# Performance work log

Hardware: AMD Instinct MI355X
Metric: run time of the kernel (lower is better)

Reference implementation:

```python
import jax, jax.numpy as jnp
import numpy as np
import math

B, N, F_IN, F_OUT = 2, 2048, 32, 32
R, LEV = 2, 2
SIGMA = 1.0


def setup_inputs() -> dict:
    key = jax.random.key(0)
    k1, k2, k3, k4 = jax.random.split(key, 4)
    x = jax.random.normal(k1, (B, N, F_IN), dtype=jnp.float32)
    # framelet decomposition operator, scaled so bmm outputs stay O(1)
    d_list = jax.random.normal(k2, (B, R * LEV * N, N + 1), dtype=jnp.float32) * (1.0 / math.sqrt(N))
    weight = jax.random.normal(k3, (F_IN, F_OUT), dtype=jnp.float32) * math.sqrt(2.0 / (F_IN + F_OUT))
    filt = jax.random.uniform(k4, (R * LEV * N, 1), dtype=jnp.float32, minval=0.9, maxval=1.1)
    bias = jnp.zeros((F_OUT,), dtype=jnp.float32)
    return {"x": x, "d_list": d_list, "weight": weight, "filt": filt, "bias": bias}


def reference(x, d_list, weight, filt, bias):
    num_nodes = x.shape[1]
    # dense feature transform
    xw = jnp.einsum('bnf,fo->bno', x, weight)
    # analysis: drop first column of d_list, bmm with transformed features
    y = d_list[:, :, 1:]                       # [B, r*Lev*N, N]
    xc = jnp.einsum('bmn,bno->bmo', y, xw)     # [B, r*Lev*N, F_OUT]
    xc = filt[None, :, :] * xc                 # learned diagonal filter
    # In the original, ms_idx is reset to 0 every loop iteration, so only
    # ms[0] (== 1.0 by construction in multiScales) is ever used as the scale.
    thr = math.sqrt(2.0 * math.log(num_nodes)) / math.sqrt(num_nodes) * SIGMA
    low = xc[:, (LEV - 1) * num_nodes:LEV * num_nodes, :]   # low-pass block, kept
    high = xc[:, LEV * num_nodes:, :]                        # high-freq blocks
    # soft threshold: sign(x)*(|x|-thr+||x|-thr|)/2 == sign(x)*relu(|x|-thr)
    high = jnp.sign(high) * jnp.maximum(jnp.abs(high) - thr, jnp.float32(0.0))
    x_shrink = jnp.concatenate([low, high], axis=1)          # [B, (r*Lev-1)*N, F_OUT]
    # synthesis: crop first node-block, raw reshape (not transpose!) as in original
    d_crop = d_list[:, num_nodes:, :]                        # [B, (r*Lev-1)*N, N+1]
    y2 = d_crop.reshape(d_crop.shape[0], num_nodes + 1, -1)  # [B, N+1, (r*Lev-1)*N]
    out = jnp.einsum('bkm,bmo->bko', y2, x_shrink) + bias    # [B, N+1, F_OUT]
    return out
```

## Files before the change

### kernel.cpp

```cpp
#include <hip/hip_runtime.h>
#include <math.h>


#define DP 2049
#define THRS 0.08628973f

typedef float  f32x4  __attribute__((ext_vector_type(4)));
typedef float  f32x16 __attribute__((ext_vector_type(16)));
typedef short  s16x8  __attribute__((ext_vector_type(8)));
typedef unsigned short u16;

#define XWT_H 0u
#define XWT_L 262144u
#define XST_H 524288u
#define XST_L 1310720u
#define P1_B  2097152u
#define P2_B  14680064u

union U8 { unsigned u[4]; s16x8 v; };

__device__ __forceinline__ unsigned cvtpk(float a, float b) {
  unsigned r;
  asm("v_cvt_pk_bf16_f32 %0, %1, %2" : "=v"(r) : "v"(a), "v"(b));
  return r;
}
__device__ __forceinline__ void split2(float a0, float a1, unsigned& h, unsigned& l) {
  h = cvtpk(a0, a1);
  const float f0 = __uint_as_float(h << 16);
  const float f1 = __uint_as_float(h & 0xFFFF0000u);
  l = cvtpk(a0 - f0, a1 - f1);
}
__device__ __forceinline__ f32x4 ld4u(const float* p) {
  f32x4 r; __builtin_memcpy(&r, p, 16); return r;
}

__global__ __launch_bounds__(256) void k_pre(const float* __restrict__ x,
                                             const float* __restrict__ wgt,
                                             u16* __restrict__ xwt_h,
                                             u16* __restrict__ xwt_l) {
  const int idx = blockIdx.x * 256 + threadIdx.x;
  const int n0  = (idx & 255) * 8;
  const int col = (idx >> 8) & 31;
  const int b   = idx >> 13;
  const float* xr = x + ((size_t)b * 2048 + n0) * 32;
  float acc[8];
#pragma unroll
  for (int j = 0; j < 8; ++j) acc[j] = 0.f;
#pragma unroll 8
  for (int f = 0; f < 32; ++f) {
    const float wf = wgt[f * 32 + col];
#pragma unroll
    for (int j = 0; j < 8; ++j) acc[j] = fmaf(xr[j * 32 + f], wf, acc[j]);
  }
  U8 H, L;
#pragma unroll
  for (int p = 0; p < 4; ++p) split2(acc[2 * p], acc[2 * p + 1], H.u[p], L.u[p]);
  const size_t o = ((size_t)b * 32 + col) * 2048 + n0;
  *(s16x8*)(xwt_h + o) = H.v;
  *(s16x8*)(xwt_l + o) = L.v;
}

__global__ __launch_bounds__(256, 4) void k_pass1(const float* __restrict__ dlist,
                                                  const u16* __restrict__ xwt_h,
                                                  const u16* __restrict__ xwt_l,
                                                  const float* __restrict__ filt,
                                                  float* __restrict__ p1) {
  const int mt = blockIdx.x, b = blockIdx.y, s = blockIdx.z;
  const int tid = threadIdx.x, wv = tid >> 6, lane = tid & 63;
  const int rc = lane & 31, oct = lane >> 5;
  const int m_a = mt * 128 + wv * 32 + rc;
  const int k0 = s * 256;

  const float* A  = dlist + ((size_t)(b * 8192 + 2048 + m_a)) * DP + 1 + k0 + oct * 8;
  const u16*   Bh = xwt_h + ((size_t)b * 32 + rc) * 2048 + k0 + oct * 8;
  const u16*   Bl = xwt_l + ((size_t)b * 32 + rc) * 2048 + k0 + oct * 8;

  f32x16 acc = {0.f,0.f,0.f,0.f,0.f,0.f,0.f,0.f,0.f,0.f,0.f,0.f,0.f,0.f,0.f,0.f};
#pragma unroll 2
  for (int st = 0; st < 16; ++st) {
    const f32x4 a0 = ld4u(A + st * 16);
    const f32x4 a1 = ld4u(A + st * 16 + 4);
    U8 Ah, Al;
    split2(a0.x, a0.y, Ah.u[0], Al.u[0]);
    split2(a0.z, a0.w, Ah.u[1], Al.u[1]);
    split2(a1.x, a1.y, Ah.u[2], Al.u[2]);
    split2(a1.z, a1.w, Ah.u[3], Al.u[3]);
    const s16x8 bh = *(const s16x8*)(Bh + st * 16);
    const s16x8 bl = *(const s16x8*)(Bl + st * 16);
    acc = __builtin_amdgcn_mfma_f32_32x32x16_bf16(Ah.v, bh, acc, 0, 0, 0);
    acc = __builtin_amdgcn_mfma_f32_32x32x16_bf16(Al.v, bh, acc, 0, 0, 0);
    acc = __builtin_amdgcn_mfma_f32_32x32x16_bf16(Ah.v, bl, acc, 0, 0, 0);
  }

  float* pc = p1 + ((size_t)((s * 2 + b) * 32 + rc)) * 6144 + mt * 128 + wv * 32 + 4 * oct;
  const float* fb = filt + 2048 + mt * 128 + wv * 32 + 4 * oct;
#pragma unroll
  for (int g = 0; g < 4; ++g) {
    const f32x4 fv = *(const f32x4*)(fb + 8 * g);
    f32x4 v;
    v.x = acc[4 * g + 0] * fv.x; v.y = acc[4 * g + 1] * fv.y;
    v.z = acc[4 * g + 2] * fv.z; v.w = acc[4 * g + 3] * fv.w;
    *(f32x4*)(pc + 8 * g) = v;
  }
}

__global__ __launch_bounds__(256) void k_shrink(const float* __restrict__ p1,
                                                u16* __restrict__ xst_h,
                                                u16* __restrict__ xst_l) {
  const int idx = blockIdx.x * 256 + threadIdx.x;
  const int m0  = (idx % 768) * 8;
  const int col = (idx / 768) % 32;
  const int b   = idx / 24576;
  f32x4 s0 = {0.f,0.f,0.f,0.f}, s1 = {0.f,0.f,0.f,0.f};
#pragma unroll
  for (int s = 0; s < 8; ++s) {
    const float* pr = p1 + ((size_t)((s * 2 + b) * 32 + col)) * 6144 + m0;
    const f32x4 v0 = *(const f32x4*)pr;
    const f32x4 v1 = *(const f32x4*)(pr + 4);
    s0 += v0; s1 += v1;
  }
  float a[8] = {s0.x, s0.y, s0.z, s0.w, s1.x, s1.y, s1.z, s1.w};
  if (m0 >= 2048) {
#pragma unroll
    for (int j = 0; j < 8; ++j) {
      const float t = fabsf(a[j]) - THRS;
      a[j] = t > 0.f ? copysignf(t, a[j]) : 0.f;
    }
  }
  U8 H, L;
#pragma unroll
  for (int p = 0; p < 4; ++p) split2(a[2 * p], a[2 * p + 1], H.u[p], L.u[p]);
  const size_t o = ((size_t)b * 32 + col) * 6144 + m0;
  *(s16x8*)(xst_h + o) = H.v;
  *(s16x8*)(xst_l + o) = L.v;
}

__global__ __launch_bounds__(256, 4) void k_pass2(const float* __restrict__ dlist,
                                                  const u16* __restrict__ xst_h,
                                                  const u16* __restrict__ xst_l,
                                                  float* __restrict__ p2) {
  const int kt = blockIdx.x, b = blockIdx.y, s = blockIdx.z;
  const int tid = threadIdx.x, wv = tid >> 6, lane = tid & 63;
  const int rc = lane & 31, oct = lane >> 5;
  int krow = kt * 128 + wv * 32 + rc;
  if (krow > 2048) krow = 2048;
  const int m0 = s * 256;

  const float* A  = dlist + (size_t)b * 8192 * DP + (size_t)2048 * DP
                  + (size_t)krow * 6144 + m0 + oct * 8;
  const u16*   Bh = xst_h + ((size_t)b * 32 + rc) * 6144 + m0 + oct * 8;
  const u16*   Bl = xst_l + ((size_t)b * 32 + rc) * 6144 + m0 + oct * 8;

  f32x16 acc = {0.f,0.f,0.f,0.f,0.f,0.f,0.f,0.f,0.f,0.f,0.f,0.f,0.f,0.f,0.f,0.f};
#pragma unroll 2
  for (int st = 0; st < 16; ++st) {
    const f32x4 a0 = *(const f32x4*)(A + st * 16);
    const f32x4 a1 = *(const f32x4*)(A + st * 16 + 4);
    U8 Ah, Al;
    split2(a0.x, a0.y, Ah.u[0], Al.u[0]);
    split2(a0.z, a0.w, Ah.u[1], Al.u[1]);
    split2(a1.x, a1.y, Ah.u[2], Al.u[2]);
    split2(a1.z, a1.w, Ah.u[3], Al.u[3]);
    const s16x8 bh = *(const s16x8*)(Bh + st * 16);
    const s16x8 bl = *(const s16x8*)(Bl + st * 16);
    acc = __builtin_amdgcn_mfma_f32_32x32x16_bf16(Ah.v, bh, acc, 0, 0, 0);
    acc = __builtin_amdgcn_mfma_f32_32x32x16_bf16(Al.v, bh, acc, 0, 0, 0);
    acc = __builtin_amdgcn_mfma_f32_32x32x16_bf16(Ah.v, bl, acc, 0, 0, 0);
  }

  float* pc = p2 + ((size_t)((s * 2 + b) * 32 + rc)) * 2176 + kt * 128 + wv * 32 + 4 * oct;
#pragma unroll
  for (int g = 0; g < 4; ++g) {
    f32x4 v;
    v.x = acc[4 * g + 0]; v.y = acc[4 * g + 1];
    v.z = acc[4 * g + 2]; v.w = acc[4 * g + 3];
    *(f32x4*)(pc + 8 * g) = v;
  }
}

__global__ __launch_bounds__(256) void k_reduce(const float* __restrict__ p2,
                                                const float* __restrict__ bias,
                                                float* __restrict__ out) {
  const int idx = blockIdx.x * 256 + threadIdx.x;
  if (idx >= 34816) return;
  const int k4  = idx % 544;
  const int col = (idx / 544) % 32;
  const int b   = idx / 17408;
  const int k0r = k4 * 4;
  f32x4 sum = {0.f,0.f,0.f,0.f};
#pragma unroll 8
  for (int s = 0; s < 24; ++s)
    sum += *(const f32x4*)(p2 + ((size_t)((s * 2 + b) * 32 + col)) * 2176 + k0r);
  const float bv = bias[col];
#pragma unroll
  for (int j = 0; j < 4; ++j) {
    const int k = k0r + j;
    if (k <= 2048) out[((size_t)b * 2049 + k) * 32 + col] = sum[j] + bv;
  }
}

extern "C" void kernel_launch(void* const* d_in, const int* in_sizes, int n_in,
                              void* d_out, int out_size, void* d_ws, size_t ws_size,
                              hipStream_t stream) {
  const float* x     = (const float*)d_in[0];
  const float* dlist = (const float*)d_in[1];
  const float* wgt   = (const float*)d_in[2];
  const float* filt  = (const float*)d_in[3];
  const float* bias  = (const float*)d_in[4];
  float* out = (float*)d_out;
  char*  ws  = (char*)d_ws;
  u16*   xwt_h = (u16*)(ws + XWT_H);
  u16*   xwt_l = (u16*)(ws + XWT_L);
  u16*   xst_h = (u16*)(ws + XST_H);
  u16*   xst_l = (u16*)(ws + XST_L);
  float* p1    = (float*)(ws + P1_B);
  float* p2    = (float*)(ws + P2_B);

  k_pre   <<<dim3(64),         dim3(256), 0, stream>>>(x, wgt, xwt_h, xwt_l);
  k_pass1 <<<dim3(48, 2, 8),   dim3(256), 0, stream>>>(dlist, xwt_h, xwt_l, filt, p1);
  k_shrink<<<dim3(192),        dim3(256), 0, stream>>>(p1, xst_h, xst_l);
  k_pass2 <<<dim3(17, 2, 24),  dim3(256), 0, stream>>>(dlist, xst_h, xst_l, p2);
  k_reduce<<<dim3(136),        dim3(256), 0, stream>>>(p2, bias, out);
}
```

Baseline: 269.5 us.

## Stage d_list tiles through LDS with async global_load_lds and packed B layout

Both GEMM passes now copy the d_list A operand into swizzled, double-buffered shared memory using global_load_lds. Each wave therefore reads rows with coalesced accesses instead of strided per-lane vector loads. The bf16 hi/lo B operands are stored pre-packed in MFMA fragment order so each lane does one contiguous load. Split-K counts rise from 8 to 16 and from 24 to 32, which adds parallelism but also makes the partial-sum reductions and workspace larger.

After: 257.8 us. -4.4%, faster.

```diff
diff --git a/kernel.cpp b/kernel.cpp
--- a/kernel.cpp
+++ b/kernel.cpp
@@ -10,12 +10,12 @@
 typedef short  s16x8  __attribute__((ext_vector_type(8)));
 typedef unsigned short u16;
 
-#define XWT_H 0u
-#define XWT_L 262144u
-#define XST_H 524288u
-#define XST_L 1310720u
+#define XWP_H 0u
+#define XWP_L 262144u
+#define XSP_H 524288u
+#define XSP_L 1310720u
 #define P1_B  2097152u
-#define P2_B  14680064u
+#define P2_B  27262976u
 
 union U8 { unsigned u[4]; s16x8 v; };
 
@@ -30,14 +30,19 @@
   const float f1 = __uint_as_float(h & 0xFFFF0000u);
   l = cvtpk(a0 - f0, a1 - f1);
 }
-__device__ __forceinline__ f32x4 ld4u(const float* p) {
-  f32x4 r; __builtin_memcpy(&r, p, 16); return r;
+__device__ __forceinline__ void cp4(const float* g, float* l) {
+  __builtin_amdgcn_global_load_lds((const __attribute__((address_space(1))) void*)g,
+                                   (__attribute__((address_space(3))) void*)l, 4, 0, 0);
+}
+__device__ __forceinline__ void cp16(const float* g, float* l) {
+  __builtin_amdgcn_global_load_lds((const __attribute__((address_space(1))) void*)g,
+                                   (__attribute__((address_space(3))) void*)l, 16, 0, 0);
 }
 
 __global__ __launch_bounds__(256) void k_pre(const float* __restrict__ x,
                                              const float* __restrict__ wgt,
-                                             u16* __restrict__ xwt_h,
-                                             u16* __restrict__ xwt_l) {
+                                             u16* __restrict__ xwp_h,
+                                             u16* __restrict__ xwp_l) {
   const int idx = blockIdx.x * 256 + threadIdx.x;
   const int n0  = (idx & 255) * 8;
   const int col = (idx >> 8) & 31;
@@ -55,41 +60,64 @@
   U8 H, L;
 #pragma unroll
   for (int p = 0; p < 4; ++p) split2(acc[2 * p], acc[2 * p + 1], H.u[p], L.u[p]);
-  const size_t o = ((size_t)b * 32 + col) * 2048 + n0;
-  *(s16x8*)(xwt_h + o) = H.v;
-  *(s16x8*)(xwt_l + o) = L.v;
+  const size_t o = (size_t)b * 65536 +
+                   ((((size_t)(n0 >> 4) * 2 + ((n0 >> 3) & 1)) * 32 + col) * 8);
+  *(s16x8*)(xwp_h + o) = H.v;
+  *(s16x8*)(xwp_l + o) = L.v;
 }
 
 __global__ __launch_bounds__(256, 4) void k_pass1(const float* __restrict__ dlist,
-                                                  const u16* __restrict__ xwt_h,
-                                                  const u16* __restrict__ xwt_l,
+                                                  const u16* __restrict__ xwp_h,
+                                                  const u16* __restrict__ xwp_l,
                                                   const float* __restrict__ filt,
                                                   float* __restrict__ p1) {
+  __shared__ float dl[2][4][1024];
   const int mt = blockIdx.x, b = blockIdx.y, s = blockIdx.z;
-  const int tid = threadIdx.x, wv = tid >> 6, lane = tid & 63;
-  const int rc = lane & 31, oct = lane >> 5;
-  const int m_a = mt * 128 + wv * 32 + rc;
-  const int k0 = s * 256;
-
-  const float* A  = dlist + ((size_t)(b * 8192 + 2048 + m_a)) * DP + 1 + k0 + oct * 8;
-  const u16*   Bh = xwt_h + ((size_t)b * 32 + rc) * 2048 + k0 + oct * 8;
-  const u16*   Bl = xwt_l + ((size_t)b * 32 + rc) * 2048 + k0 + oct * 8;
+  const int tid = threadIdx.x, wv = tid >> 6, l = tid & 63;
+  const int rc = l & 31, oct = l >> 5;
+  const int k0 = s * 128;
+
+  const int cl = ((l >> 2) & 7) ^ (l >> 5);
+  const float* dbase = dlist +
+      ((size_t)(b * 8192 + 2048 + mt * 128 + wv * 32 + (l >> 5))) * DP + 1 + k0 + (l & 3);
+
+  const u16* Bh = xwp_h + (size_t)b * 65536;
+  const u16* Bl = xwp_l + (size_t)b * 65536;
+
+  auto stage = [&](int buf, int kc) {
+    float* lb = &dl[buf][wv][0];
+#pragma unroll 4
+    for (int i = 0; i < 16; ++i)
+      cp4(dbase + (size_t)(2 * i) * DP + kc + ((cl ^ ((2 * i) & 7)) << 2), lb + i * 64);
+  };
 
   f32x16 acc = {0.f,0.f,0.f,0.f,0.f,0.f,0.f,0.f,0.f,0.f,0.f,0.f,0.f,0.f,0.f,0.f};
-#pragma unroll 2
-  for (int st = 0; st < 16; ++st) {
-    const f32x4 a0 = ld4u(A + st * 16);
-    const f32x4 a1 = ld4u(A + st * 16 + 4);
-    U8 Ah, Al;
-    split2(a0.x, a0.y, Ah.u[0], Al.u[0]);
-    split2(a0.z, a0.w, Ah.u[1], Al.u[1]);
-    split2(a1.x, a1.y, Ah.u[2], Al.u[2]);
-    split2(a1.z, a1.w, Ah.u[3], Al.u[3]);
-    const s16x8 bh = *(const s16x8*)(Bh + st * 16);
-    const s16x8 bl = *(const s16x8*)(Bl + st * 16);
-    acc = __builtin_amdgcn_mfma_f32_32x32x16_bf16(Ah.v, bh, acc, 0, 0, 0);
-    acc = __builtin_amdgcn_mfma_f32_32x32x16_bf16(Al.v, bh, acc, 0, 0, 0);
-    acc = __builtin_amdgcn_mfma_f32_32x32x16_bf16(Ah.v, bl, acc, 0, 0, 0);
+
+  stage(0, 0);
+#pragma unroll 1
+  for (int c = 0; c < 4; ++c) {
+    __syncthreads();
+    if (c < 3) stage((c + 1) & 1, (c + 1) * 32);
+    const float* wb = &dl[c & 1][wv][0];
+#pragma unroll
+    for (int st = 0; st < 2; ++st) {
+      const int T = s * 8 + c * 2 + st;
+      const int s0 = (4 * st + 2 * oct) ^ (rc & 7);
+      const int s1 = (4 * st + 2 * oct + 1) ^ (rc & 7);
+      const f32x4 a0 = *(const f32x4*)(wb + rc * 32 + s0 * 4);
+      const f32x4 a1 = *(const f32x4*)(wb + rc * 32 + s1 * 4);
+      U8 Ah, Al;
+      split2(a0.x, a0.y, Ah.u[0], Al.u[0]);
+      split2(a0.z, a0.w, Ah.u[1], Al.u[1]);
+      split2(a1.x, a1.y, Ah.u[2], Al.u[2]);
+      split2(a1.z, a1.w, Ah.u[3], Al.u[3]);
+      const size_t bo = ((size_t)(T * 2 + oct) * 32 + rc) * 8;
+      const s16x8 bh = *(const s16x8*)(Bh + bo);
+      const s16x8 bl = *(const s16x8*)(Bl + bo);
+      acc = __builtin_amdgcn_mfma_f32_32x32x16_bf16(Ah.v, bh, acc, 0, 0, 0);
+      acc = __builtin_amdgcn_mfma_f32_32x32x16_bf16(Al.v, bh, acc, 0, 0, 0);
+      acc = __builtin_amdgcn_mfma_f32_32x32x16_bf16(Ah.v, bl, acc, 0, 0, 0);
+    }
   }
 
   float* pc = p1 + ((size_t)((s * 2 + b) * 32 + rc)) * 6144 + mt * 128 + wv * 32 + 4 * oct;
@@ -105,19 +133,18 @@
 }
 
 __global__ __launch_bounds__(256) void k_shrink(const float* __restrict__ p1,
-                                                u16* __restrict__ xst_h,
-                                                u16* __restrict__ xst_l) {
+                                                u16* __restrict__ xsp_h,
+                                                u16* __restrict__ xsp_l) {
   const int idx = blockIdx.x * 256 + threadIdx.x;
   const int m0  = (idx % 768) * 8;
   const int col = (idx / 768) % 32;
   const int b   = idx / 24576;
   f32x4 s0 = {0.f,0.f,0.f,0.f}, s1 = {0.f,0.f,0.f,0.f};
 #pragma unroll
-  for (int s = 0; s < 8; ++s) {
+  for (int s = 0; s < 16; ++s) {
     const float* pr = p1 + ((size_t)((s * 2 + b) * 32 + col)) * 6144 + m0;
-    const f32x4 v0 = *(const f32x4*)pr;
-    const f32x4 v1 = *(const f32x4*)(pr + 4);
-    s0 += v0; s1 += v1;
+    s0 += *(const f32x4*)pr;
+    s1 += *(const f32x4*)(pr + 4);
   }
   float a[8] = {s0.x, s0.y, s0.z, s0.w, s1.x, s1.y, s1.z, s1.w};
   if (m0 >= 2048) {
@@ -130,42 +157,66 @@
   U8 H, L;
 #pragma unroll
   for (int p = 0; p < 4; ++p) split2(a[2 * p], a[2 * p + 1], H.u[p], L.u[p]);
-  const size_t o = ((size_t)b * 32 + col) * 6144 + m0;
-  *(s16x8*)(xst_h + o) = H.v;
-  *(s16x8*)(xst_l + o) = L.v;
+  const size_t o = (size_t)b * 196608 +
+                   ((((size_t)(m0 >> 4) * 2 + ((m0 >> 3) & 1)) * 32 + col) * 8);
+  *(s16x8*)(xsp_h + o) = H.v;
+  *(s16x8*)(xsp_l + o) = L.v;
 }
 
 __global__ __launch_bounds__(256, 4) void k_pass2(const float* __restrict__ dlist,
-                                                  const u16* __restrict__ xst_h,
-                                                  const u16* __restrict__ xst_l,
+                                                  const u16* __restrict__ xsp_h,
+                                                  const u16* __restrict__ xsp_l,
                                                   float* __restrict__ p2) {
+  __shared__ float dl[2][4][1024];
   const int kt = blockIdx.x, b = blockIdx.y, s = blockIdx.z;
-  const int tid = threadIdx.x, wv = tid >> 6, lane = tid & 63;
-  const int rc = lane & 31, oct = lane >> 5;
-  int krow = kt * 128 + wv * 32 + rc;
-  if (krow > 2048) krow = 2048;
-  const int m0 = s * 256;
-
-  const float* A  = dlist + (size_t)b * 8192 * DP + (size_t)2048 * DP
-                  + (size_t)krow * 6144 + m0 + oct * 8;
-  const u16*   Bh = xst_h + ((size_t)b * 32 + rc) * 6144 + m0 + oct * 8;
-  const u16*   Bl = xst_l + ((size_t)b * 32 + rc) * 6144 + m0 + oct * 8;
+  const int tid = threadIdx.x, wv = tid >> 6, l = tid & 63;
+  const int rc = l & 31, oct = l >> 5;
+  const int m0 = s * 192;
+
+  const int row_l = kt * 128 + wv * 32 + (l >> 3);
+  const int swz = (l & 7) ^ ((l >> 3) & 7);
+  const float* Ab = dlist + (size_t)b * 8192 * DP + (size_t)2048 * DP + m0 + swz * 4;
+
+  const u16* Bh = xsp_h + (size_t)b * 196608;
+  const u16* Bl = xsp_l + (size_t)b * 196608;
+
+  auto stage = [&](int buf, int kc) {
+    float* lb = &dl[buf][wv][0];
+#pragma unroll
+    for (int i = 0; i < 4; ++i) {
+      int rg = row_l + 8 * i;
+      rg = rg > 2048 ? 2048 : rg;
+      cp16(Ab + (size_t)rg * 6144 + kc, lb + i * 256);
+    }
+  };
 
   f32x16 acc = {0.f,0.f,0.f,0.f,0.f,0.f,0.f,0.f,0.f,0.f,0.f,0.f,0.f,0.f,0.f,0.f};
-#pragma unroll 2
-  for (int st = 0; st < 16; ++st) {
-    const f32x4 a0 = *(const f32x4*)(A + st * 16);
-    const f32x4 a1 = *(const f32x4*)(A + st * 16 + 4);
-    U8 Ah, Al;
-    split2(a0.x, a0.y, Ah.u[0], Al.u[0]);
-    split2(a0.z, a0.w, Ah.u[1], Al.u[1]);
-    split2(a1.x, a1.y, Ah.u[2], Al.u[2]);
-    split2(a1.z, a1.w, Ah.u[3], Al.u[3]);
-    const s16x8 bh = *(const s16x8*)(Bh + st * 16);
-    const s16x8 bl = *(const s16x8*)(Bl + st * 16);
-    acc = __builtin_amdgcn_mfma_f32_32x32x16_bf16(Ah.v, bh, acc, 0, 0, 0);
-    acc = __builtin_amdgcn_mfma_f32_32x32x16_bf16(Al.v, bh, acc, 0, 0, 0);
-    acc = __builtin_amdgcn_mfma_f32_32x32x16_bf16(Ah.v, bl, acc, 0, 0, 0);
+
+  stage(0, 0);
+#pragma unroll 1
+  for (int c = 0; c < 6; ++c) {
+    __syncthreads();
+    if (c < 5) stage((c + 1) & 1, (c + 1) * 32);
+    const float* wb = &dl[c & 1][wv][0];
+#pragma unroll
+    for (int st = 0; st < 2; ++st) {
+      const int T = s * 12 + c * 2 + st;
+      const int s0 = (4 * st + 2 * oct) ^ (rc & 7);
+      const int s1 = (4 * st + 2 * oct + 1) ^ (rc & 7);
+      const f32x4 a0 = *(const f32x4*)(wb + rc * 32 + s0 * 4);
+      const f32x4 a1 = *(const f32x4*)(wb + rc * 32 + s1 * 4);
+      U8 Ah, Al;
+      split2(a0.x, a0.y, Ah.u[0], Al.u[0]);
+      split2(a0.z, a0.w, Ah.u[1], Al.u[1]);
+      split2(a1.x, a1.y, Ah.u[2], Al.u[2]);
+      split2(a1.z, a1.w, Ah.u[3], Al.u[3]);
+      const size_t bo = ((size_t)(T * 2 + oct) * 32 + rc) * 8;
+      const s16x8 bh = *(const s16x8*)(Bh + bo);
+      const s16x8 bl = *(const s16x8*)(Bl + bo);
+      acc = __builtin_amdgcn_mfma_f32_32x32x16_bf16(Ah.v, bh, acc, 0, 0, 0);
+      acc = __builtin_amdgcn_mfma_f32_32x32x16_bf16(Al.v, bh, acc, 0, 0, 0);
+      acc = __builtin_amdgcn_mfma_f32_32x32x16_bf16(Ah.v, bl, acc, 0, 0, 0);
+    }
   }
 
   float* pc = p2 + ((size_t)((s * 2 + b) * 32 + rc)) * 2176 + kt * 128 + wv * 32 + 4 * oct;
@@ -189,7 +240,7 @@
   const int k0r = k4 * 4;
   f32x4 sum = {0.f,0.f,0.f,0.f};
 #pragma unroll 8
-  for (int s = 0; s < 24; ++s)
+  for (int s = 0; s < 32; ++s)
     sum += *(const f32x4*)(p2 + ((size_t)((s * 2 + b) * 32 + col)) * 2176 + k0r);
   const float bv = bias[col];
 #pragma unroll
@@ -209,16 +260,16 @@
   const float* bias  = (const float*)d_in[4];
   float* out = (float*)d_out;
   char*  ws  = (char*)d_ws;
-  u16*   xwt_h = (u16*)(ws + XWT_H);
-  u16*   xwt_l = (u16*)(ws + XWT_L);
-  u16*   xst_h = (u16*)(ws + XST_H);
-  u16*   xst_l = (u16*)(ws + XST_L);
+  u16*   xwp_h = (u16*)(ws + XWP_H);
+  u16*   xwp_l = (u16*)(ws + XWP_L);
+  u16*   xsp_h = (u16*)(ws + XSP_H);
+  u16*   xsp_l = (u16*)(ws + XSP_L);
   float* p1    = (float*)(ws + P1_B);
   float* p2    = (float*)(ws + P2_B);
 
-  k_pre   <<<dim3(64),         dim3(256), 0, stream>>>(x, wgt, xwt_h, xwt_l);
-  k_pass1 <<<dim3(48, 2, 8),   dim3(256), 0, stream>>>(dlist, xwt_h, xwt_l, filt, p1);
-  k_shrink<<<dim3(192),        dim3(256), 0, stream>>>(p1, xst_h, xst_l);
-  k_pass2 <<<dim3(17, 2, 24),  dim3(256), 0, stream>>>(dlist, xst_h, xst_l, p2);
+  k_pre   <<<dim3(64),         dim3(256), 0, stream>>>(x, wgt, xwp_h, xwp_l);
+  k_pass1 <<<dim3(48, 2, 16),  dim3(256), 0, stream>>>(dlist, xwp_h, xwp_l, filt, p1);
+  k_shrink<<<dim3(192),        dim3(256), 0, stream>>>(p1, xsp_h, xsp_l);
+  k_pass2 <<<dim3(17, 2, 32),  dim3(256), 0, stream>>>(dlist, xsp_h, xsp_l, p2);
   k_reduce<<<dim3(136),        dim3(256), 0, stream>>>(p2, bias, out);
 }
```
